# Optimization experiments

Measured on AMD Instinct MI355X. Metric: run time of the kernel, lower is better.

The kernel has to match this reference:

```python
import jax, jax.numpy as jnp
import numpy as np

ATOM = 8          # atom_size
STRIDE = 4
NB_ATOMS = 256
LMBDA = 0.1       # l1 prox weight (prox_params)
NONDIFF = 20      # nondiff_steps (run under stop_gradient, mirroring torch.no_grad)
DIFF = 5          # diff_steps


def setup_inputs() -> dict:
    key = jax.random.key(0)
    k1, k2 = jax.random.split(key)
    y = jax.random.normal(k1, (8, 3, 256, 256), dtype=jnp.float32)
    # atoms ~ N(0,1)/sqrt(nb_channels*atom_size^2), as in __init__ with init='random'
    atoms = jax.random.normal(k2, (NB_ATOMS, 3, ATOM, ATOM), dtype=jnp.float32) / np.float32(np.sqrt(3 * ATOM * ATOM))
    return {"y": y, "atoms": atoms}


def _forward(y, atoms):
    B, C, H, W = y.shape
    a, s = ATOM, STRIDE
    Hp = (H - a) // s + 1
    Wp = (W - a) // s + 1
    D = C * a * a

    # patch row/col index grids: rows[ph, i] = ph*s + i
    rows = (jnp.arange(Hp) * s)[:, None] + jnp.arange(a)          # [Hp, a]
    cols = (jnp.arange(Wp) * s)[:, None] + jnp.arange(a)          # [Wp, a]
    R4 = rows[:, :, None, None]                                    # [Hp, a, 1, 1]
    C4 = cols[None, None, :, :]                                    # [1, 1, Wp, a]

    # unfold: extract overlapping patches -> [B, C, Hp, a, Wp, a] -> [N, D] (channel-major, matching torch)
    p6 = y[:, :, R4, C4]
    p = p6.transpose(0, 2, 4, 1, 3, 5).reshape(B * Hp * Wp, D)     # N = B*Hp*Wp

    mean = jnp.mean(p, axis=1, keepdims=True)                      # per-patch mean
    p = p - mean

    # l2-normalize atoms
    A = atoms.reshape(NB_ATOMS, D)
    A = A / jnp.linalg.norm(A, axis=1, keepdims=True)              # [nA, D]

    X = A @ A.T                                                    # [nA, nA] Gram matrix
    q = A @ p.T                                                    # [nA, N]
    L = jnp.linalg.norm(X, 2)                                      # spectral norm (Lipschitz const)
    thr = LMBDA / L

    def ista_step(c, _):
        c = c - (X @ c - q) / L
        c = jnp.sign(c) * jnp.maximum(jnp.abs(c) - thr, 0.0)       # soft-threshold prox
        return c, None

    c0 = jnp.zeros((NB_ATOMS, q.shape[1]), dtype=q.dtype)
    c, _ = jax.lax.scan(ista_step, c0, None, length=NONDIFF)
    c = jax.lax.stop_gradient(c)                                    # torch.no_grad() warmup
    c, _ = jax.lax.scan(ista_step, c, None, length=DIFF)

    # reconstruct patches: einsum('ij,il->jl') = c.T @ A, add mean back
    rec = c.T @ A + mean                                            # [N, D]
    p6r = rec.reshape(B, Hp, Wp, C, a, a).transpose(0, 3, 1, 4, 2, 5)  # [B, C, Hp, a, Wp, a]

    # fold: overlap-add patches back to image
    out = jnp.zeros((B, C, H, W), dtype=y.dtype).at[:, :, R4, C4].add(p6r)
    counts = jnp.zeros((H, W), dtype=y.dtype).at[R4, C4].add(
        jnp.ones((Hp, a, Wp, a), dtype=y.dtype))                    # overlap divisors
    return out / counts


def reference(y, atoms):
    return _forward(y, atoms)
```

## Files before the change

kernel.cpp:

```cpp
#include <hip/hip_runtime.h>
#include <math.h>

#define NPATCH 31752
#define TILE   64
#define PSTR   200
#define MSTR   200

typedef _Float16 f16;
typedef __attribute__((ext_vector_type(2))) _Float16 f16x2;
typedef __attribute__((ext_vector_type(4))) _Float16 f16x4;
typedef __attribute__((ext_vector_type(8))) _Float16 f16x8;
typedef __attribute__((ext_vector_type(2))) __fp16   hf16x2;
typedef __attribute__((ext_vector_type(4))) float    f32x4;
#define MFMA16 __builtin_amdgcn_mfma_f32_16x16x32_f16

union HU { f16x2 h; hf16x2 g; unsigned u; };

__device__ __forceinline__ f16x2 pk2(float a, float b)
{
    HU r; r.g = __builtin_amdgcn_cvt_pkrtz(a, b);
    return r.h;
}

__device__ __forceinline__ f16x2 shrink2(f16x2 v, f16x2 thr2)
{
    HU a; a.h = v;
    unsigned sgn = a.u & 0x80008000u;
    a.u &= 0x7FFF7FFFu;
    f16x2 t = a.h - thr2;
    t = __builtin_elementwise_max(t, (f16x2)(f16)0);
    HU r; r.h = t; r.u |= sgn;
    return r.h;
}

__global__ void fusedpack_kernel(const float* __restrict__ atoms,
                                 float* __restrict__ A, float* __restrict__ As,
                                 f16* __restrict__ Ap, f16* __restrict__ Ab)
{
    __shared__ float part[6];
    const int b = blockIdx.x, t = threadIdx.x;
    float v = atoms[b*192 + t];
    float s = v*v, r = v;
    #pragma unroll
    for (int m = 1; m < 64; m <<= 1) { s += __shfl_xor(s, m, 64); r += __shfl_xor(r, m, 64); }
    const int wv = t >> 6, lane = t & 63;
    if (lane == 0) { part[wv] = s; part[3 + wv] = r; }
    __syncthreads();
    s = part[0] + part[1] + part[2];
    r = part[3] + part[4] + part[5];
    float rn = 1.0f / sqrtf(s);
    float a  = v * rn;
    A[b*192 + t] = a;
    if (t == 0) As[b] = r * rn;
    f16 ah = (f16)a;
    {
        int I = b >> 4, l16 = b & 15;
        int ks = t >> 5, q = (t >> 3) & 3, j = t & 7;
        Ap[(((I*6 + ks)*64) + q*16 + l16)*8 + j] = ah;
    }
    {
        int dt = t >> 4, dl = t & 15;
        int ks = b >> 5, q = (b >> 3) & 3, j = b & 7;
        Ab[(((dt*8 + ks)*64) + q*16 + dl)*8 + j] = ah;
    }
}

__global__ __launch_bounds__(256, 1)
void lchain_kernel(const f16* __restrict__ Ab, float* __restrict__ scal)
{
    __shared__ f16   mls[2 * 192 * MSTR];
    __shared__ float red[4];
    __shared__ float trc[16];
    const int tid = threadIdx.x, wv = tid >> 6, lane = tid & 63;
    const int quad = lane >> 4, l16 = lane & 15;
    const f16x8* AbV = (const f16x8*)Ab;

    f32x4 acc[3][12];
    #pragma unroll
    for (int it = 0; it < 3; ++it)
        #pragma unroll
        for (int J = 0; J < 12; ++J) acc[it][J] = (f32x4){0,0,0,0};
    for (int ks = 0; ks < 8; ++ks) {
        f16x8 bf[12];
        #pragma unroll
        for (int J = 0; J < 12; ++J) bf[J] = AbV[(J*8 + ks)*64 + lane];
        #pragma unroll
        for (int it = 0; it < 3; ++it) {
            f16x8 af = AbV[((3*wv + it)*8 + ks)*64 + lane];
            #pragma unroll
            for (int J = 0; J < 12; ++J)
                acc[it][J] = MFMA16(af, bf[J], acc[it][J], 0, 0, 0);
        }
    }
    #pragma unroll
    for (int it = 0; it < 3; ++it) {
        int I = 3*wv + it;
        #pragma unroll
        for (int J = 0; J < 12; ++J) {
            f16x2 lo = pk2(acc[it][J][0], acc[it][J][1]);
            f16x2 hi = pk2(acc[it][J][2], acc[it][J][3]);
            f16x4 cc; cc[0]=lo[0]; cc[1]=lo[1]; cc[2]=hi[0]; cc[3]=hi[1];
            *(f16x4*)&mls[(J*16 + l16)*MSTR + I*16 + quad*4] = cc;
        }
    }
    __syncthreads();

    float rprev = 1.0f;
    for (int t = 1; t <= 8; ++t) {
        const f16* src = mls + ((t & 1) ^ 1) * (192 * MSTR);
        f16*       dst = mls + (t & 1) * (192 * MSTR);
        const float inv = 1.0f / rprev;
        const float inv2 = inv * inv;

        f32x4 a2[3][12];
        #pragma unroll
        for (int it = 0; it < 3; ++it)
            #pragma unroll
            for (int J = 0; J < 12; ++J) a2[it][J] = (f32x4){0,0,0,0};
        for (int ks = 0; ks < 6; ++ks) {
            f16x8 bf[12];
            #pragma unroll
            for (int J = 0; J < 12; ++J)
                bf[J] = *(const f16x8*)&src[(J*16 + l16)*MSTR + ks*32 + quad*8];
            #pragma unroll
            for (int it = 0; it < 3; ++it) {
                f16x8 af = *(const f16x8*)&src[((3*wv + it)*16 + l16)*MSTR + ks*32 + quad*8];
                #pragma unroll
                for (int J = 0; J < 12; ++J)
                    a2[it][J] = MFMA16(af, bf[J], a2[it][J], 0, 0, 0);
            }
        }
        float dsum = 0.0f;
        #pragma unroll
        for (int it = 0; it < 3; ++it) {
            int I = 3*wv + it;
            #pragma unroll
            for (int J = 0; J < 12; ++J) {
                float v0 = a2[it][J][0] * inv2;
                float v1 = a2[it][J][1] * inv2;
                float v2 = a2[it][J][2] * inv2;
                float v3 = a2[it][J][3] * inv2;
                f16x2 lo = pk2(v0, v1);
                f16x2 hi = pk2(v2, v3);
                f16x4 cc; cc[0]=lo[0]; cc[1]=lo[1]; cc[2]=hi[0]; cc[3]=hi[1];
                *(f16x4*)&dst[(J*16 + l16)*MSTR + I*16 + quad*4] = cc;
                if (J == I) {
                    int dg = l16 - quad*4;
                    if (dg >= 0 && dg < 4)
                        dsum += (dg == 0 ? v0 : dg == 1 ? v1 : dg == 2 ? v2 : v3);
                }
            }
        }
        #pragma unroll
        for (int m = 1; m < 64; m <<= 1) dsum += __shfl_xor(dsum, m, 64);
        if (lane == 0) red[wv] = dsum;
        __syncthreads();
        float r = red[0] + red[1] + red[2] + red[3];
        if (tid == 0) trc[t] = r;
        rprev = r;
        __syncthreads();
    }
    if (tid == 0) {
        float a = 0.0f;
        #pragma unroll
        for (int u = 1; u <= 8; ++u) a += exp2f(-(float)u) * log2f(trc[u]);
        float L = exp2f(a);
        scal[16] = 1.0f / L;
        scal[17] = 0.1f / L;
    }
}

__global__ void gpack_kernel(const float* __restrict__ A, const float* __restrict__ scal,
                             f16* __restrict__ Gp)
{
    __shared__ float arow[192];
    __shared__ float xrow[256];
    int i = blockIdx.x, j = threadIdx.x;
    const float invL = scal[16];
    if (j < 192) arow[j] = A[i*192 + j];
    __syncthreads();
    float s = 0.0f;
    #pragma unroll 4
    for (int d = 0; d < 192; d += 4) {
        float4 av = *(const float4*)&A[j*192 + d];
        s += arow[d]*av.x + arow[d+1]*av.y + arow[d+2]*av.z + arow[d+3]*av.w;
    }
    xrow[j] = (i == j ? 1.0f : 0.0f) - s * invL;
    __syncthreads();
    if (j < 32) {
        int ks = j >> 2, q = j & 3;
        f16x8 h;
        #pragma unroll
        for (int u = 0; u < 8; ++u) h[u] = (f16)xrow[ks*32 + q*8 + u];
        int I = i >> 4, lane = q*16 + (i & 15);
        *(f16x8*)&Gp[(((I*8 + ks)*64) + lane)*8] = h;
    }
}

__global__ __launch_bounds__(256, 2)
void mega_kernel(const float* __restrict__ y,
                 const f16* __restrict__ Gp, const f16* __restrict__ Ap,
                 const f16* __restrict__ Ab, const float* __restrict__ As,
                 const float* __restrict__ scal, float* __restrict__ out)
{
    __shared__ f16      p_lds[TILE * PSTR];
    __shared__ f16      c_lds[2 * 16 * 512];
    __shared__ float    mean_lds[TILE];
    __shared__ float    msum[512];
    __shared__ unsigned pco[TILE];

    const int tid  = threadIdx.x;
    const int base = blockIdx.x * TILE;
    const int wv = tid >> 6, lane = tid & 63, quad = lane >> 4, l16 = lane & 15;
    const float invL = scal[16];
    const float thr  = scal[17];
    const f16x2 thr2 = { (f16)thr, (f16)thr };

    #define CWADDR(st, rt, ct) \
        ((st)*8192 + ((ct)*8 + (wv*2 + ((rt)>>1)))*512 \
         + ((((rt)&1)*2 + (quad>>1))*16 + l16)*8 + (quad&1)*4)

    f16x8 greg[4][8];
    {
        const f16x8* GpV = (const f16x8*)Gp;
        #pragma unroll
        for (int rt = 0; rt < 4; ++rt)
            #pragma unroll
            for (int ks = 0; ks < 8; ++ks)
                greg[rt][ks] = GpV[((wv*4 + rt)*8 + ks)*64 + lane];
    }

    #pragma unroll
    for (int p = 0; p < 2; ++p) {
        int n_l = p*32 + (tid >> 3), qq = tid & 7;
        int n = base + n_l; if (n >= NPATCH) n = NPATCH - 1;
        int b = n / 3969, rem = n - b * 3969;
        int r = rem / 63, sc = rem - r * 63;
        if (qq == 0) pco[n_l] = ((unsigned)b << 16) | ((unsigned)r << 8) | (unsigned)sc;
        float s = 0.0f;
        #pragma unroll
        for (int u = 0; u < 3; ++u) {
            int d  = qq * 24 + u * 8;
            int ch = d >> 6, id = (d & 63) >> 3;
            const float* src = &y[((b*3 + ch)*256 + (r*4 + id))*256 + sc*4];
            float4 a = *(const float4*)src;
            float4 bq = *(const float4*)(src + 4);
            s += a.x + a.y + a.z + a.w + bq.x + bq.y + bq.z + bq.w;
            f16x8 h = { (f16)a.x, (f16)a.y, (f16)a.z, (f16)a.w,
                        (f16)bq.x, (f16)bq.y, (f16)bq.z, (f16)bq.w };
            *(f16x8*)&p_lds[n_l * PSTR + d] = h;
        }
        msum[p*256 + tid] = s;
    }
    __syncthreads();
    if (tid < TILE) {
        int p = tid >> 5, bse = (tid & 31) * 8;
        float s = 0.0f;
        #pragma unroll
        for (int u = 0; u < 8; ++u) s += msum[p*256 + bse + u];
        mean_lds[tid] = s * (1.0f / 192.0f);
    }
    __syncthreads();

    f16x2 qslo[2][4][2], qshi[2][4][2];
    const f16x8* ApV = (const f16x8*)Ap;
    #pragma unroll
    for (int st = 0; st < 2; ++st) {
        f32x4 qf[4][2];
        #pragma unroll
        for (int rt = 0; rt < 4; ++rt)
            #pragma unroll
            for (int ct = 0; ct < 2; ++ct) qf[rt][ct] = (f32x4){0,0,0,0};
        #pragma unroll
        for (int ks = 0; ks < 6; ++ks) {
            f16x8 bf[2];
            #pragma unroll
            for (int ct = 0; ct < 2; ++ct)
                bf[ct] = *(const f16x8*)&p_lds[(st*32 + ct*16 + l16)*PSTR + ks*32 + quad*8];
            #pragma unroll
            for (int rt = 0; rt < 4; ++rt) {
                f16x8 af = ApV[((wv*4 + rt)*6 + ks)*64 + lane];
                #pragma unroll
                for (int ct = 0; ct < 2; ++ct)
                    qf[rt][ct] = MFMA16(af, bf[ct], qf[rt][ct], 0, 0, 0);
            }
        }
        #pragma unroll
        for (int rt = 0; rt < 4; ++rt) {
            float a0 = As[wv*64 + rt*16 + quad*4 + 0];
            float a1 = As[wv*64 + rt*16 + quad*4 + 1];
            float a2 = As[wv*64 + rt*16 + quad*4 + 2];
            float a3 = As[wv*64 + rt*16 + quad*4 + 3];
            #pragma unroll
            for (int ct = 0; ct < 2; ++ct) {
                float mn = mean_lds[st*32 + ct*16 + l16];
                float q0 = (qf[rt][ct][0] - mn*a0) * invL;
                float q1 = (qf[rt][ct][1] - mn*a1) * invL;
                float q2 = (qf[rt][ct][2] - mn*a2) * invL;
                float q3 = (qf[rt][ct][3] - mn*a3) * invL;
                f16x2 lo = pk2(q0, q1);
                f16x2 hi = pk2(q2, q3);
                qslo[st][rt][ct] = lo;  qshi[st][rt][ct] = hi;
                f16x2 clo = shrink2(lo, thr2);
                f16x2 chi = shrink2(hi, thr2);
                f16x4 cc; cc[0]=clo[0]; cc[1]=clo[1]; cc[2]=chi[0]; cc[3]=chi[1];
                *(f16x4*)&c_lds[CWADDR(st, rt, ct)] = cc;
            }
        }
    }
    __syncthreads();

    for (int it = 0; it < 24; ++it) {
        f32x4 af[4][2];
        #pragma unroll
        for (int rt = 0; rt < 4; ++rt)
            #pragma unroll
            for (int ct = 0; ct < 2; ++ct) af[rt][ct] = (f32x4){0,0,0,0};
        #pragma unroll
        for (int ks = 0; ks < 8; ++ks) {
            f16x8 b0 = *(const f16x8*)&c_lds[(ks)*512 + lane*8];
            f16x8 b1 = *(const f16x8*)&c_lds[(8 + ks)*512 + lane*8];
            #pragma unroll
            for (int rt = 0; rt < 4; ++rt) {
                af[rt][0] = MFMA16(greg[rt][ks], b0, af[rt][0], 0, 0, 0);
                af[rt][1] = MFMA16(greg[rt][ks], b1, af[rt][1], 0, 0, 0);
            }
        }
        __syncthreads();
        #pragma unroll
        for (int rt = 0; rt < 4; ++rt)
            #pragma unroll
            for (int ct = 0; ct < 2; ++ct) {
                f16x2 vlo = pk2(af[rt][ct][0], af[rt][ct][1]) + qslo[0][rt][ct];
                f16x2 vhi = pk2(af[rt][ct][2], af[rt][ct][3]) + qshi[0][rt][ct];
                vlo = shrink2(vlo, thr2);
                vhi = shrink2(vhi, thr2);
                f16x4 cc; cc[0]=vlo[0]; cc[1]=vlo[1]; cc[2]=vhi[0]; cc[3]=vhi[1];
                *(f16x4*)&c_lds[CWADDR(0, rt, ct)] = cc;
            }
        #pragma unroll
        for (int rt = 0; rt < 4; ++rt)
            #pragma unroll
            for (int ct = 0; ct < 2; ++ct) af[rt][ct] = (f32x4){0,0,0,0};
        #pragma unroll
        for (int ks = 0; ks < 8; ++ks) {
            f16x8 b0 = *(const f16x8*)&c_lds[8192 + (ks)*512 + lane*8];
            f16x8 b1 = *(const f16x8*)&c_lds[8192 + (8 + ks)*512 + lane*8];
            #pragma unroll
            for (int rt = 0; rt < 4; ++rt) {
                af[rt][0] = MFMA16(greg[rt][ks], b0, af[rt][0], 0, 0, 0);
                af[rt][1] = MFMA16(greg[rt][ks], b1, af[rt][1], 0, 0, 0);
            }
        }
        __syncthreads();
        #pragma unroll
        for (int rt = 0; rt < 4; ++rt)
            #pragma unroll
            for (int ct = 0; ct < 2; ++ct) {
                f16x2 vlo = pk2(af[rt][ct][0], af[rt][ct][1]) + qslo[1][rt][ct];
                f16x2 vhi = pk2(af[rt][ct][2], af[rt][ct][3]) + qshi[1][rt][ct];
                vlo = shrink2(vlo, thr2);
                vhi = shrink2(vhi, thr2);
                f16x4 cc; cc[0]=vlo[0]; cc[1]=vlo[1]; cc[2]=vhi[0]; cc[3]=vhi[1];
                *(f16x4*)&c_lds[CWADDR(1, rt, ct)] = cc;
            }
    }
    __syncthreads();

    const int nt = wv >> 1, dtb = 6 * (wv & 1);
    const f16x8* AbV = (const f16x8*)Ab;
    #pragma unroll
    for (int st = 0; st < 2; ++st) {
        f32x4 rf[6];
        #pragma unroll
        for (int u = 0; u < 6; ++u) rf[u] = (f32x4){0,0,0,0};
        #pragma unroll
        for (int ks = 0; ks < 8; ++ks) {
            f16x8 afr = *(const f16x8*)&c_lds[st*8192 + (nt*8 + ks)*512 + lane*8];
            #pragma unroll
            for (int u = 0; u < 6; ++u) {
                f16x8 bb = AbV[((dtb + u)*8 + ks)*64 + lane];
                rf[u] = MFMA16(afr, bb, rf[u], 0, 0, 0);
            }
        }
        #pragma unroll
        for (int g = 0; g < 4; ++g) {
            int nl = nt*16 + quad*4 + g;
            int n  = base + st*32 + nl;
            if (n < NPATCH) {
                unsigned pc = pco[st*32 + nl];
                int b = pc >> 16, r = (pc >> 8) & 255, sc = pc & 255;
                float mn = mean_lds[st*32 + nl];
                #pragma unroll
                for (int u = 0; u < 6; ++u) {
                    int d  = (dtb + u)*16 + l16;
                    int ch = d >> 6, dh = (d & 63) >> 3, dw = d & 7;
                    atomicAdd(&out[((b*3 + ch)*256 + (r*4 + dh))*256 + sc*4 + dw],
                              rf[u][g] + mn);
                }
            }
        }
    }
    #undef CWADDR
}

__global__ void divcnt_kernel(float* __restrict__ out)
{
    int idx = blockIdx.x * 256 + threadIdx.x;
    int w = idx & 255, h = (idx >> 8) & 255;
    int rlo = max(h - 4, 0) >> 2, rhi = min(62, h >> 2);
    int slo = max(w - 4, 0) >> 2, shi = min(62, w >> 2);
    out[idx] *= 1.0f / (float)((rhi - rlo + 1) * (shi - slo + 1));
}

extern "C" void kernel_launch(void* const* d_in, const int* in_sizes, int n_in,
                              void* d_out, int out_size, void* d_ws, size_t ws_size,
                              hipStream_t stream)
{
    const float* y     = (const float*)d_in[0];
    const float* atoms = (const float*)d_in[1];
    float* out = (float*)d_out;
    float* ws  = (float*)d_ws;

    float* A    = ws;
    float* As   = ws + 49152;
    float* scal = ws + 49408;
    f16*   Ap   = (f16*)(ws + 49440);
    f16*   Ab   = (f16*)(ws + 74016);
    f16*   Gp   = (f16*)(ws + 98592);

    (void)hipMemsetAsync(d_out, 0, (size_t)out_size * sizeof(float), stream);

    fusedpack_kernel<<<256, 192, 0, stream>>>(atoms, A, As, Ap, Ab);
    lchain_kernel   <<<1, 256,   0, stream>>>(Ab, scal);
    gpack_kernel    <<<256, 256, 0, stream>>>(A, scal, Gp);
    mega_kernel     <<<(NPATCH + TILE - 1) / TILE, 256, 0, stream>>>
        (y, Gp, Ap, Ab, As, scal, out);
    divcnt_kernel   <<<6144, 256, 0, stream>>>(out);
}
```

Measured before the change: 218.9 us.

## Spread spectral-norm squaring chain over many blocks and fold count division into scatter

Replaces the single-block fp16 MFMA repeated-squaring kernel for the Lipschitz constant with per-step fp32 matrix-square kernels that run across 256 blocks, followed by a small finalize kernel. The chain goes one squaring deeper and accumulates diagonal traces with atomics. The separate divide-by-overlap-count pass is removed by scaling each atomic contribution in the scatter. The cost is about nine extra kernel launches, fp32 scalar-loop matmuls, and extra per-element divide arithmetic in the mega kernel.

```diff
diff --git a/kernel.cpp b/kernel.cpp
--- a/kernel.cpp
+++ b/kernel.cpp
@@ -4,7 +4,6 @@
 #define NPATCH 31752
 #define TILE   64
 #define PSTR   200
-#define MSTR   200
 
 typedef _Float16 f16;
 typedef __attribute__((ext_vector_type(2))) _Float16 f16x2;
@@ -35,10 +34,12 @@
 
 __global__ void fusedpack_kernel(const float* __restrict__ atoms,
                                  float* __restrict__ A, float* __restrict__ As,
-                                 f16* __restrict__ Ap, f16* __restrict__ Ab)
+                                 f16* __restrict__ Ap, f16* __restrict__ Ab,
+                                 float* __restrict__ scal)
 {
     __shared__ float part[6];
     const int b = blockIdx.x, t = threadIdx.x;
+    if (b == 0 && t < 32) scal[t] = 0.0f;
     float v = atoms[b*192 + t];
     float s = v*v, r = v;
     #pragma unroll
@@ -65,118 +66,10 @@
     }
 }
 
-__global__ __launch_bounds__(256, 1)
-void lchain_kernel(const f16* __restrict__ Ab, float* __restrict__ scal)
-{
-    __shared__ f16   mls[2 * 192 * MSTR];
-    __shared__ float red[4];
-    __shared__ float trc[16];
-    const int tid = threadIdx.x, wv = tid >> 6, lane = tid & 63;
-    const int quad = lane >> 4, l16 = lane & 15;
-    const f16x8* AbV = (const f16x8*)Ab;
-
-    f32x4 acc[3][12];
-    #pragma unroll
-    for (int it = 0; it < 3; ++it)
-        #pragma unroll
-        for (int J = 0; J < 12; ++J) acc[it][J] = (f32x4){0,0,0,0};
-    for (int ks = 0; ks < 8; ++ks) {
-        f16x8 bf[12];
-        #pragma unroll
-        for (int J = 0; J < 12; ++J) bf[J] = AbV[(J*8 + ks)*64 + lane];
-        #pragma unroll
-        for (int it = 0; it < 3; ++it) {
-            f16x8 af = AbV[((3*wv + it)*8 + ks)*64 + lane];
-            #pragma unroll
-            for (int J = 0; J < 12; ++J)
-                acc[it][J] = MFMA16(af, bf[J], acc[it][J], 0, 0, 0);
-        }
-    }
-    #pragma unroll
-    for (int it = 0; it < 3; ++it) {
-        int I = 3*wv + it;
-        #pragma unroll
-        for (int J = 0; J < 12; ++J) {
-            f16x2 lo = pk2(acc[it][J][0], acc[it][J][1]);
-            f16x2 hi = pk2(acc[it][J][2], acc[it][J][3]);
-            f16x4 cc; cc[0]=lo[0]; cc[1]=lo[1]; cc[2]=hi[0]; cc[3]=hi[1];
-            *(f16x4*)&mls[(J*16 + l16)*MSTR + I*16 + quad*4] = cc;
-        }
-    }
-    __syncthreads();
-
-    float rprev = 1.0f;
-    for (int t = 1; t <= 8; ++t) {
-        const f16* src = mls + ((t & 1) ^ 1) * (192 * MSTR);
-        f16*       dst = mls + (t & 1) * (192 * MSTR);
-        const float inv = 1.0f / rprev;
-        const float inv2 = inv * inv;
-
-        f32x4 a2[3][12];
-        #pragma unroll
-        for (int it = 0; it < 3; ++it)
-            #pragma unroll
-            for (int J = 0; J < 12; ++J) a2[it][J] = (f32x4){0,0,0,0};
-        for (int ks = 0; ks < 6; ++ks) {
-            f16x8 bf[12];
-            #pragma unroll
-            for (int J = 0; J < 12; ++J)
-                bf[J] = *(const f16x8*)&src[(J*16 + l16)*MSTR + ks*32 + quad*8];
-            #pragma unroll
-            for (int it = 0; it < 3; ++it) {
-                f16x8 af = *(const f16x8*)&src[((3*wv + it)*16 + l16)*MSTR + ks*32 + quad*8];
-                #pragma unroll
-                for (int J = 0; J < 12; ++J)
-                    a2[it][J] = MFMA16(af, bf[J], a2[it][J], 0, 0, 0);
-            }
-        }
-        float dsum = 0.0f;
-        #pragma unroll
-        for (int it = 0; it < 3; ++it) {
-            int I = 3*wv + it;
-            #pragma unroll
-            for (int J = 0; J < 12; ++J) {
-                float v0 = a2[it][J][0] * inv2;
-                float v1 = a2[it][J][1] * inv2;
-                float v2 = a2[it][J][2] * inv2;
-                float v3 = a2[it][J][3] * inv2;
-                f16x2 lo = pk2(v0, v1);
-                f16x2 hi = pk2(v2, v3);
-                f16x4 cc; cc[0]=lo[0]; cc[1]=lo[1]; cc[2]=hi[0]; cc[3]=hi[1];
-                *(f16x4*)&dst[(J*16 + l16)*MSTR + I*16 + quad*4] = cc;
-                if (J == I) {
-                    int dg = l16 - quad*4;
-                    if (dg >= 0 && dg < 4)
-                        dsum += (dg == 0 ? v0 : dg == 1 ? v1 : dg == 2 ? v2 : v3);
-                }
-            }
-        }
-        #pragma unroll
-        for (int m = 1; m < 64; m <<= 1) dsum += __shfl_xor(dsum, m, 64);
-        if (lane == 0) red[wv] = dsum;
-        __syncthreads();
-        float r = red[0] + red[1] + red[2] + red[3];
-        if (tid == 0) trc[t] = r;
-        rprev = r;
-        __syncthreads();
-    }
-    if (tid == 0) {
-        float a = 0.0f;
-        #pragma unroll
-        for (int u = 1; u <= 8; ++u) a += exp2f(-(float)u) * log2f(trc[u]);
-        float L = exp2f(a);
-        scal[16] = 1.0f / L;
-        scal[17] = 0.1f / L;
-    }
-}
-
-__global__ void gpack_kernel(const float* __restrict__ A, const float* __restrict__ scal,
-                             f16* __restrict__ Gp)
+__global__ void x_kernel(const float* __restrict__ A, float* __restrict__ X)
 {
     __shared__ float arow[192];
-    __shared__ float xrow[256];
     int i = blockIdx.x, j = threadIdx.x;
-    const float invL = scal[16];
     if (j < 192) arow[j] = A[i*192 + j];
     __syncthreads();
     float s = 0.0f;
@@ -185,7 +78,44 @@
         float4 av = *(const float4*)&A[j*192 + d];
         s += arow[d]*av.x + arow[d+1]*av.y + arow[d+2]*av.z + arow[d+3]*av.w;
     }
-    xrow[j] = (i == j ? 1.0f : 0.0f) - s * invL;
+    X[i*256 + j] = s;
+}
+
+__global__ void sq_kernel(const float* __restrict__ Min, float* __restrict__ Mout,
+                          float* __restrict__ scal, int tprev, int tcur)
+{
+    __shared__ float row[256];
+    int i = blockIdx.x, j = threadIdx.x;
+    float inv = tprev ? (1.0f / scal[tprev]) : 1.0f;
+    row[j] = Min[i*256 + j];
+    __syncthreads();
+    float s = 0.0f;
+    #pragma unroll 4
+    for (int k = 0; k < 256; ++k) s += row[k] * Min[k*256 + j];
+    float val = s * inv * inv;
+    Mout[i*256 + j] = val;
+    if (j == i) atomicAdd(&scal[tcur], val);
+}
+
+__global__ void lfin_kernel(float* scal)
+{
+    if (threadIdx.x == 0) {
+        float a = 0.0f;
+        #pragma unroll
+        for (int u = 1; u <= 9; ++u) a += exp2f(-(float)u) * log2f(scal[u]);
+        float L = exp2f(a);
+        scal[16] = 1.0f / L;
+        scal[17] = 0.1f / L;
+    }
+}
+
+__global__ void gpack_kernel(const float* __restrict__ X, const float* __restrict__ scal,
+                             f16* __restrict__ Gp)
+{
+    __shared__ float xrow[256];
+    int i = blockIdx.x, j = threadIdx.x;
+    const float invL = scal[16];
+    xrow[j] = (i == j ? 1.0f : 0.0f) - X[i*256 + j] * invL;
     __syncthreads();
     if (j < 32) {
         int ks = j >> 2, q = j & 3;
@@ -395,22 +325,17 @@
                 for (int u = 0; u < 6; ++u) {
                     int d  = (dtb + u)*16 + l16;
                     int ch = d >> 6, dh = (d & 63) >> 3, dw = d & 7;
+                    int h  = r*4 + dh, w2 = sc*4 + dw;
+                    int cnth = min(62, h >> 2)  - (max(h - 4, 0) >> 2) + 1;
+                    int cntw = min(62, w2 >> 2) - (max(w2 - 4, 0) >> 2) + 1;
+                    float rcp = 1.0f / (float)(cnth * cntw);
                     atomicAdd(&out[((b*3 + ch)*256 + (r*4 + dh))*256 + sc*4 + dw],
-                              rf[u][g] + mn);
+                              (rf[u][g] + mn) * rcp);
                 }
             }
         }
     }
     #undef CWADDR
-}
-
-__global__ void divcnt_kernel(float* __restrict__ out)
-{
-    int idx = blockIdx.x * 256 + threadIdx.x;
-    int w = idx & 255, h = (idx >> 8) & 255;
-    int rlo = max(h - 4, 0) >> 2, rhi = min(62, h >> 2);
-    int slo = max(w - 4, 0) >> 2, shi = min(62, w >> 2);
-    out[idx] *= 1.0f / (float)((rhi - rlo + 1) * (shi - slo + 1));
 }
 
 extern "C" void kernel_launch(void* const* d_in, const int* in_sizes, int n_in,
@@ -428,13 +353,24 @@
     f16*   Ap   = (f16*)(ws + 49440);
     f16*   Ab   = (f16*)(ws + 74016);
     f16*   Gp   = (f16*)(ws + 98592);
+    float* X    = ws + 131360;
+    float* M0   = ws + 196896;
+    float* M1   = ws + 262432;
 
     (void)hipMemsetAsync(d_out, 0, (size_t)out_size * sizeof(float), stream);
 
-    fusedpack_kernel<<<256, 192, 0, stream>>>(atoms, A, As, Ap, Ab);
-    lchain_kernel   <<<1, 256,   0, stream>>>(Ab, scal);
-    gpack_kernel    <<<256, 256, 0, stream>>>(A, scal, Gp);
-    mega_kernel     <<<(NPATCH + TILE - 1) / TILE, 256, 0, stream>>>
+    fusedpack_kernel<<<256, 192, 0, stream>>>(atoms, A, As, Ap, Ab, scal);
+    x_kernel        <<<256, 256, 0, stream>>>(A, X);
+
+    const float* src = X;
+    float* dst = M0;
+    for (int t = 1; t <= 9; ++t) {
+        sq_kernel<<<256, 256, 0, stream>>>(src, dst, scal, t - 1, t);
+        src = dst;
+        dst = (dst == M0) ? M1 : M0;
+    }
+    lfin_kernel <<<1, 64,    0, stream>>>(scal);
+    gpack_kernel<<<256, 256, 0, stream>>>(X, scal, Gp);
+    mega_kernel <<<(NPATCH + TILE - 1) / TILE, 256, 0, stream>>>
         (y, Gp, Ap, Ab, As, scal, out);
-    divcnt_kernel   <<<6144, 256, 0, stream>>>(out);
-}
+}
```

Result: slower. 368.2 us (+68.2%).
